# Kernel optimization log

Hardware: AMD Instinct MI355X
Metric: run time of the kernel (lower is better)

The kernel has to match this reference:

```python
import jax, jax.numpy as jnp
import numpy as np
from jax import lax

DT = 1.0 / 120.0
B, T = 4096, 128
TWO_PI = 2.0 * np.pi


def setup_inputs() -> dict:
    key = jax.random.key(0)
    k1, k2, k3, k4 = jax.random.split(key, 4)
    return {
        "params": jax.random.normal(k1, (4,), jnp.float32),
        "covariance_params": jax.random.normal(k2, (7,), jnp.float32),
        "init_states": jax.random.normal(k3, (B, 6), jnp.float32),
        "measurements": jax.random.normal(k4, (B, T, 3), jnp.float32),
    }


def _wrap(a):
    # wrap angle innovation to [-pi, pi]
    return a - TWO_PI * jnp.round(a / TWO_PI)


def _smooth_loss(params, covariance_params, init_state, z):
    # z: [T, 3] measurements of (x, y, theta)
    friction = (jnp.tanh(params[0]) + 1.0) * 0.01
    damping = (jnp.tanh(params[1]) + 1.0) * 0.01
    cp = jax.nn.sigmoid(covariance_params)
    R = jnp.diag(cp[:3])                                    # [3,3] meas noise
    Q = jnp.diag(cp[jnp.array([3, 3, 4, 4, 5, 6])])         # [6,6] proc noise
    I6 = jnp.eye(6, dtype=z.dtype)
    Hm = jnp.zeros((3, 6), z.dtype).at[0, 0].set(1.).at[1, 1].set(1.).at[2, 4].set(1.)
    P0 = 0.01 * I6

    def f_and_F(s):
        # free-sliding puck dynamics: [x, y, dx, dy, th, dth]
        x, y, dx, dy, th, dth = s
        ndx = dx - DT * (damping * dx + friction * jnp.tanh(100. * dx))
        ndy = dy - DT * (damping * dy + friction * jnp.tanh(100. * dy))
        ndth = dth * (1.0 - DT * damping)
        ns = jnp.stack([x + DT * dx, y + DT * dy, ndx, ndy, th + DT * dth, ndth])
        gx = 1.0 - DT * (damping + friction * 100. * (1. - jnp.tanh(100. * dx) ** 2))
        gy = 1.0 - DT * (damping + friction * 100. * (1. - jnp.tanh(100. * dy) ** 2))
        F = (I6.at[0, 2].set(DT).at[1, 3].set(DT).at[4, 5].set(DT)
               .at[2, 2].set(gx).at[3, 3].set(gy).at[5, 5].set(1.0 - DT * damping))
        return ns, F

    def ekf_step(carry, zt):
        s, P = carry
        sp, F = f_and_F(s)
        Pp = F @ P @ F.T + Q
        S = Hm @ Pp @ Hm.T + R
        innov = zt - Hm @ sp
        innov = innov.at[2].set(_wrap(innov[2]))
        K = jnp.linalg.solve(S, Hm @ Pp).T          # Pp H^T S^-1
        s_new = sp + K @ innov
        P_new = (I6 - K @ Hm) @ Pp
        return (s_new, P_new), (s_new, P_new, sp, Pp, F)

    _, (sf, Pf, sp, Pp, Fs) = lax.scan(ekf_step, (init_state, P0), z)

    # RTS backward pass
    def rts_step(carry, inp):
        s_next, P_next = carry
        s_f, P_f, sp_n, Pp_n, F_n = inp
        G = jnp.linalg.solve(Pp_n, F_n @ P_f).T     # P_f F^T Pp^{-1}
        s_s = s_f + G @ (s_next - sp_n)
        P_s = P_f + G @ (P_next - Pp_n) @ G.T
        return (s_s, P_s), (s_s, P_s)

    inp = (sf[:-1], Pf[:-1], sp[1:], Pp[1:], Fs[1:])
    _, (s_sm_head, P_sm_head) = lax.scan(rts_step, (sf[-1], Pf[-1]), inp, reverse=True)
    s_sm = jnp.concatenate([s_sm_head, sf[-1:]], 0)   # [T,6]
    P_sm = jnp.concatenate([P_sm_head, Pf[-1:]], 0)   # [T,6,6]

    # log-lik style loss vs measurements[2:] (as in compute_loss)
    zz, st, Pt = z[2:], s_sm[2:], P_sm[2:]
    Sv = jnp.einsum('ij,tjk,lk->til', Hm, Pt, Hm) + R  # [T-2,3,3] meas-space var
    innov_xy = zz[:, :2] - st[:, :2]
    a = zz[:, 2] - st[:, 4]
    a = jnp.where(a > 1.5 * np.pi, a - TWO_PI, a)
    a = jnp.where(a < -1.5 * np.pi, a + TWO_PI, a)
    innov = jnp.concatenate([innov_xy, a[:, None]], 1)
    sign, logdet = jnp.linalg.slogdet(Sv)
    return jnp.sum(sign * jnp.exp(logdet) + jnp.einsum('ti,tij,tj->t', innov, Sv, innov))


def reference(params, covariance_params, init_states, measurements):
    per_seg = jax.vmap(_smooth_loss, in_axes=(None, None, 0, 0))(
        params, covariance_params, init_states, measurements)
    return jnp.sum(per_seg)
```

## Files before the change

### kernel.cpp

```cpp
#include <hip/hip_runtime.h>
#include <cmath>


namespace {

constexpr int B = 4096;
constexpr int T = 128;
constexpr int SPB = 64;
constexpr int NBLK = B / SPB;
constexpr int NTH = 3 * SPB;
constexpr int NT = B * 3;
constexpr float DTc     = 1.0f / 120.0f;
constexpr float TWO_PIc = 6.28318530717958647692f;
constexpr float PI_1_5  = 4.71238898038468985769f;
constexpr float INV_2PI = 0.15915494309189533577f;

__device__ __forceinline__ float frcp(float x) { return __builtin_amdgcn_rcpf(x); }

__device__ __forceinline__ float fast_tanh(float x) {
  float e = __expf(2.0f * x);
  return 1.0f - 2.0f * frcp(e + 1.0f);
}
__device__ __forceinline__ float sigmoidf(float x) {
  return frcp(1.0f + __expf(-x));
}

__global__ __launch_bounds__(NTH, 1) void fused_kernel(
    const float* __restrict__ params, const float* __restrict__ covp,
    const float* __restrict__ init_states, const float* __restrict__ z,
    float4* __restrict__ hist4, float* __restrict__ hist1,
    float2* __restrict__ aq, float* __restrict__ out) {
  const int tid = threadIdx.x;
  const int f = tid >> 6;
  const int sb = tid & 63;
  const int blk = blockIdx.x;
  const int seq = blk * SPB + sb;
  const int gid = blk * NTH + tid;

  __shared__ float zl[384 * 65];
  __shared__ float red[3];

  {
    const float* __restrict__ zslab = z + (size_t)blk * SPB * (T * 3);
    const int q = (tid >= 96) ? 1 : 0;
    const int col = (tid - q * 96) * 4;
#pragma unroll 4
    for (int i = 0; i < 32; i++) {
      const int s2 = i * 2 + q;
      const float4 v4 = *(const float4*)(zslab + (size_t)i * 768 + tid * 4);
      zl[(col + 0) * 65 + s2] = v4.x;
      zl[(col + 1) * 65 + s2] = v4.y;
      zl[(col + 2) * 65 + s2] = v4.z;
      zl[(col + 3) * 65 + s2] = v4.w;
    }
  }
  __syncthreads();

  const float friction = (fast_tanh(params[0]) + 1.0f) * 0.01f;
  const float damping  = (fast_tanh(params[1]) + 1.0f) * 0.01f;
  float cp[7];
#pragma unroll
  for (int i = 0; i < 7; i++) cp[i] = sigmoidf(covp[i]);
  const float dcoef = 1.0f - DTc * damping;
  const bool isTH = (f == 2);
  const float q0 = isTH ? cp[5] : cp[3];
  const float q1 = isTH ? cp[6] : cp[4];
  const float r  = cp[f];

  const int pidx = (f == 0) ? 0 : (f == 1) ? 1 : 4;
  const int vidx = (f == 0) ? 2 : (f == 1) ? 3 : 5;
  float p = init_states[seq * 6 + pidx];
  float v = init_states[seq * 6 + vidx];
  float P00 = 0.01f, P01 = 0.0f, P11 = 0.01f;

#pragma unroll 8
  for (int t = 0; t < T; t++) {
    const float zc = zl[(t * 3 + f) * 65 + sb];

    float g, tv;
    if (!isTH) {
      const float th = fast_tanh(100.0f * v);
      tv = v - DTc * (damping * v + friction * th);
      g = 1.0f - DTc * (damping + 100.0f * friction * (1.0f - th * th));
    } else {
      tv = dcoef * v;
      g = dcoef;
    }
    const float tp = p + DTc * v;
    const float u = P01 + DTc * P11;
    const float Pp00 = P00 + DTc * P01 + DTc * u + q0;
    const float Pp01 = g * u;
    const float Pp11 = g * (g * P11) + q1;
    const float iS = frcp(Pp00 + r);
    const float K0 = Pp00 * iS;
    const float K1 = Pp01 * iS;
    float e = zc - tp;
    if (isTH) e = e - TWO_PIc * rintf(e * INV_2PI);
    p = tp + K0 * e;
    v = tv + K1 * e;
    const float om = 1.0f - K0;
    P00 = om * Pp00;
    P01 = om * Pp01;
    P11 = Pp11 - K1 * Pp01;

    hist4[(size_t)t * NT + gid] = make_float4(p, v, P00, P01);
    hist1[(size_t)t * NT + gid] = P11;
  }

  {
    const float zlv = zl[((T - 1) * 3 + f) * 65 + sb];
    float e = zlv - p;
    if (isTH) {
      if (e >  PI_1_5) e -= TWO_PIc;
      if (e < -PI_1_5) e += TWO_PIc;
    }
    const float a = P00 + r;
    aq[(size_t)(T - 1) * NT + gid] = make_float2(a, a * e * e);
  }

  float sp_ = p, sv_ = v, Ps00 = P00, Ps01 = P01, Ps11 = P11;

  float4 h4b[8];
  float h1b[8];
#pragma unroll
  for (int i = 0; i < 8; i++) {
    const int n2 = 126 - i;
    h4b[i] = hist4[(size_t)n2 * NT + gid];
    h1b[i] = hist1[(size_t)n2 * NT + gid];
  }

#pragma unroll 8
  for (int i = 0; i < 128; i++) {
    const int n = 126 - i;
    const int sl = i & 7;
    const float4 h4 = h4b[sl];
    const float h1 = h1b[sl];
    const int nz = (n < 2) ? 2 : n;
    const float zn_ = zl[(nz * 3 + f) * 65 + sb];
    const int nf = (n >= 10) ? (n - 8) : 2;
    h4b[sl] = hist4[(size_t)nf * NT + gid];
    h1b[sl] = hist1[(size_t)nf * NT + gid];

    const float fp = h4.x, fv = h4.y, f00 = h4.z, f01 = h4.w, f11 = h1;

    float g, tv;
    if (!isTH) {
      const float th = fast_tanh(100.0f * fv);
      tv = fv - DTc * (damping * fv + friction * th);
      g = 1.0f - DTc * (damping + 100.0f * friction * (1.0f - th * th));
    } else {
      tv = dcoef * fv;
      g = dcoef;
    }
    const float tp = fp + DTc * fv;
    const float u = f01 + DTc * f11;
    const float Pp00 = f00 + DTc * f01 + DTc * u + q0;
    const float Pp01 = g * u;
    const float Pp11 = g * (g * f11) + q1;

    const float idet = frcp(Pp00 * Pp11 - Pp01 * Pp01);
    const float W00 = f00, W01 = DTc * f00 + g * f01;
    const float W10 = f01, W11 = DTc * f01 + g * f11;
    const float G00 = (W00 * Pp11 - W01 * Pp01) * idet;
    const float G01 = (W01 * Pp00 - W00 * Pp01) * idet;
    const float G10 = (W10 * Pp11 - W11 * Pp01) * idet;
    const float G11 = (W11 * Pp00 - W10 * Pp01) * idet;

    const float ds0 = sp_ - tp, ds1 = sv_ - tv;
    const float np = fp + G00 * ds0 + G01 * ds1;
    const float nv = fv + G10 * ds0 + G11 * ds1;

    const float M00 = Ps00 - Pp00, M01 = Ps01 - Pp01, M11 = Ps11 - Pp11;
    const float GM00 = G00 * M00 + G01 * M01, GM01 = G00 * M01 + G01 * M11;
    const float GM10 = G10 * M00 + G11 * M01, GM11 = G10 * M01 + G11 * M11;
    Ps00 = f00 + GM00 * G00 + GM01 * G01;
    Ps01 = f01 + GM00 * G10 + GM01 * G11;
    Ps11 = f11 + GM10 * G10 + GM11 * G11;
    sp_ = np;
    sv_ = nv;

    if (n >= 2) {
      const float a = Ps00 + r;
      float e = zn_ - np;
      if (isTH) {
        if (e >  PI_1_5) e -= TWO_PIc;
        if (e < -PI_1_5) e += TWO_PIc;
      }
      aq[(size_t)n * NT + gid] = make_float2(a, a * e * e);
    }
  }

  __syncthreads();

  float part = 0.0f;
  const int base = blk * NTH;

  float2 b0[4], b1[4], b2[4];
#pragma unroll
  for (int k = 0; k < 4; k++) {
    const int pi = tid + k * NTH;
    const size_t o = (size_t)(2 + (pi >> 6)) * NT + base + (pi & 63);
    b0[k] = aq[o];
    b1[k] = aq[o + 64];
    b2[k] = aq[o + 128];
  }

#pragma unroll 4
  for (int k = 0; k < 44; k++) {
    const int sl = k & 3;
    const float2 x0 = b0[sl];
    const float2 x1 = b1[sl];
    const float2 x2 = b2[sl];
    const int kf = (k + 4 < 42) ? (k + 4) : 41;
    {
      const int pi = tid + kf * NTH;
      const size_t o = (size_t)(2 + (pi >> 6)) * NT + base + (pi & 63);
      b0[sl] = aq[o];
      b1[sl] = aq[o + 64];
      b2[sl] = aq[o + 128];
    }
    if (k < 42) part += x0.x * x1.x * x2.x + (x0.y + x1.y + x2.y);
  }

#pragma unroll
  for (int off = 32; off > 0; off >>= 1) part += __shfl_down(part, off);
  if ((tid & 63) == 0) red[tid >> 6] = part;
  __syncthreads();
  if (tid == 0) atomicAdd(out, red[0] + red[1] + red[2]);
}

}

extern "C" void kernel_launch(void* const* d_in, const int* in_sizes, int n_in,
                              void* d_out, int out_size, void* d_ws, size_t ws_size,
                              hipStream_t stream) {
  const float* params      = (const float*)d_in[0];
  const float* covp        = (const float*)d_in[1];
  const float* init_states = (const float*)d_in[2];
  const float* z           = (const float*)d_in[3];
  float* out = (float*)d_out;

  const size_t hist4B = (size_t)T * NT * sizeof(float4);
  const size_t hist1B = (size_t)T * NT * sizeof(float);
  const size_t aqB    = (size_t)T * NT * sizeof(float2);
  const size_t needBytes = hist4B + hist1B + aqB;

  hipMemsetAsync(d_out, 0, sizeof(float), stream);

  if (ws_size >= needBytes) {
    float4* hist4 = (float4*)d_ws;
    float*  hist1 = (float*)((char*)d_ws + hist4B);
    float2* aqp   = (float2*)((char*)d_ws + hist4B + hist1B);
    fused_kernel<<<NBLK, NTH, 0, stream>>>(params, covp, init_states, z,
                                           hist4, hist1, aqp, out);
  }
}
```

Before: 121.9 us.

## Split filter into one-wave blocks with LDS history and separate reduction kernel

Restructures the work so each 64-thread block handles one coordinate channel for 64 sequences, giving 192 blocks instead of 64. The float4 filter history now lives in shared memory rather than global workspace, and measurements are read straight from global memory instead of being transposed into LDS. The final loss reduction moves to a separate grid-stride kernel. The aim is better CU occupancy and less global history traffic, at the cost of an extra kernel launch, strided uncoalesced z reads, and 128 KB of LDS per block.

```diff
diff --git a/kernel.cpp b/kernel.cpp
--- a/kernel.cpp
+++ b/kernel.cpp
@@ -6,10 +6,12 @@
 
 constexpr int B = 4096;
 constexpr int T = 128;
-constexpr int SPB = 64;
-constexpr int NBLK = B / SPB;
-constexpr int NTH = 3 * SPB;
 constexpr int NT = B * 3;
+constexpr int CPB = 64;
+constexpr int NBLK = NT / CPB;
+constexpr int RBLK = 256;
+constexpr int RTH = 256;
+
 constexpr float DTc     = 1.0f / 120.0f;
 constexpr float TWO_PIc = 6.28318530717958647692f;
 constexpr float PI_1_5  = 4.71238898038468985769f;
@@ -25,36 +27,17 @@
   return frcp(1.0f + __expf(-x));
 }
 
-__global__ __launch_bounds__(NTH, 1) void fused_kernel(
+__global__ __launch_bounds__(CPB, 1) void filt_kernel(
     const float* __restrict__ params, const float* __restrict__ covp,
     const float* __restrict__ init_states, const float* __restrict__ z,
-    float4* __restrict__ hist4, float* __restrict__ hist1,
-    float2* __restrict__ aq, float* __restrict__ out) {
-  const int tid = threadIdx.x;
-  const int f = tid >> 6;
-  const int sb = tid & 63;
-  const int blk = blockIdx.x;
-  const int seq = blk * SPB + sb;
-  const int gid = blk * NTH + tid;
-
-  __shared__ float zl[384 * 65];
-  __shared__ float red[3];
-
-  {
-    const float* __restrict__ zslab = z + (size_t)blk * SPB * (T * 3);
-    const int q = (tid >= 96) ? 1 : 0;
-    const int col = (tid - q * 96) * 4;
-#pragma unroll 4
-    for (int i = 0; i < 32; i++) {
-      const int s2 = i * 2 + q;
-      const float4 v4 = *(const float4*)(zslab + (size_t)i * 768 + tid * 4);
-      zl[(col + 0) * 65 + s2] = v4.x;
-      zl[(col + 1) * 65 + s2] = v4.y;
-      zl[(col + 2) * 65 + s2] = v4.z;
-      zl[(col + 3) * 65 + s2] = v4.w;
-    }
-  }
-  __syncthreads();
+    float* __restrict__ hist1, float2* __restrict__ aq) {
+  const int lane = threadIdx.x;
+  const int blk  = blockIdx.x;
+  const int f    = blk >> 6;
+  const int seq  = ((blk & 63) << 6) + lane;
+  const int gid  = blk * CPB + lane;
+
+  __shared__ float4 h4s[T * CPB];
 
   const float friction = (fast_tanh(params[0]) + 1.0f) * 0.01f;
   const float damping  = (fast_tanh(params[1]) + 1.0f) * 0.01f;
@@ -73,9 +56,11 @@
   float v = init_states[seq * 6 + vidx];
   float P00 = 0.01f, P01 = 0.0f, P11 = 0.01f;
 
+  const float* __restrict__ zp = z + (size_t)seq * (T * 3) + f;
+
 #pragma unroll 8
   for (int t = 0; t < T; t++) {
-    const float zc = zl[(t * 3 + f) * 65 + sb];
+    const float zc = zp[t * 3];
 
     float g, tv;
     if (!isTH) {
@@ -103,45 +88,38 @@
     P01 = om * Pp01;
     P11 = Pp11 - K1 * Pp01;
 
-    hist4[(size_t)t * NT + gid] = make_float4(p, v, P00, P01);
+    h4s[t * CPB + lane] = make_float4(p, v, P00, P01);
     hist1[(size_t)t * NT + gid] = P11;
   }
 
   {
-    const float zlv = zl[((T - 1) * 3 + f) * 65 + sb];
-    float e = zlv - p;
+    float e = zp[(T - 1) * 3] - p;
     if (isTH) {
       if (e >  PI_1_5) e -= TWO_PIc;
       if (e < -PI_1_5) e += TWO_PIc;
     }
     const float a = P00 + r;
-    aq[(size_t)(T - 1) * NT + gid] = make_float2(a, a * e * e);
+    aq[((size_t)f * T + (T - 1)) * B + seq] = make_float2(a, a * e * e);
   }
 
   float sp_ = p, sv_ = v, Ps00 = P00, Ps01 = P01, Ps11 = P11;
 
-  float4 h4b[8];
   float h1b[8];
 #pragma unroll
-  for (int i = 0; i < 8; i++) {
-    const int n2 = 126 - i;
-    h4b[i] = hist4[(size_t)n2 * NT + gid];
-    h1b[i] = hist1[(size_t)n2 * NT + gid];
-  }
+  for (int i = 0; i < 8; i++) h1b[i] = hist1[(size_t)(126 - i) * NT + gid];
 
 #pragma unroll 8
   for (int i = 0; i < 128; i++) {
     const int n = 126 - i;
+    const int nc = (n < 2) ? 2 : n;
     const int sl = i & 7;
-    const float4 h4 = h4b[sl];
-    const float h1 = h1b[sl];
-    const int nz = (n < 2) ? 2 : n;
-    const float zn_ = zl[(nz * 3 + f) * 65 + sb];
+    const float4 h4 = h4s[nc * CPB + lane];
+    const float f11 = h1b[sl];
     const int nf = (n >= 10) ? (n - 8) : 2;
-    h4b[sl] = hist4[(size_t)nf * NT + gid];
     h1b[sl] = hist1[(size_t)nf * NT + gid];
-
-    const float fp = h4.x, fv = h4.y, f00 = h4.z, f01 = h4.w, f11 = h1;
+    const float zn_ = zp[nc * 3];
+
+    const float fp = h4.x, fv = h4.y, f00 = h4.z, f01 = h4.w;
 
     float g, tv;
     if (!isTH) {
@@ -186,47 +164,35 @@
         if (e >  PI_1_5) e -= TWO_PIc;
         if (e < -PI_1_5) e += TWO_PIc;
       }
-      aq[(size_t)n * NT + gid] = make_float2(a, a * e * e);
-    }
-  }
-
-  __syncthreads();
-
+      aq[((size_t)f * T + n) * B + seq] = make_float2(a, a * e * e);
+    }
+  }
+}
+
+__global__ __launch_bounds__(RTH) void reduce_kernel(
+    const float2* __restrict__ aq, float* __restrict__ out) {
+  const int tid = threadIdx.x;
+  constexpr int NTERM = 126 * B;
   float part = 0.0f;
-  const int base = blk * NTH;
-
-  float2 b0[4], b1[4], b2[4];
-#pragma unroll
-  for (int k = 0; k < 4; k++) {
-    const int pi = tid + k * NTH;
-    const size_t o = (size_t)(2 + (pi >> 6)) * NT + base + (pi & 63);
-    b0[k] = aq[o];
-    b1[k] = aq[o + 64];
-    b2[k] = aq[o + 128];
-  }
-
-#pragma unroll 4
-  for (int k = 0; k < 44; k++) {
-    const int sl = k & 3;
-    const float2 x0 = b0[sl];
-    const float2 x1 = b1[sl];
-    const float2 x2 = b2[sl];
-    const int kf = (k + 4 < 42) ? (k + 4) : 41;
-    {
-      const int pi = tid + kf * NTH;
-      const size_t o = (size_t)(2 + (pi >> 6)) * NT + base + (pi & 63);
-      b0[sl] = aq[o];
-      b1[sl] = aq[o + 64];
-      b2[sl] = aq[o + 128];
-    }
-    if (k < 42) part += x0.x * x1.x * x2.x + (x0.y + x1.y + x2.y);
-  }
-
+  for (int idx = blockIdx.x * RTH + tid; idx < NTERM; idx += RTH * RBLK) {
+    const int t = 2 + (idx >> 12);
+    const int s = idx & (B - 1);
+    const float2 a0 = aq[((size_t)0 * T + t) * B + s];
+    const float2 a1 = aq[((size_t)1 * T + t) * B + s];
+    const float2 a2 = aq[((size_t)2 * T + t) * B + s];
+    part += a0.x * a1.x * a2.x + (a0.y + a1.y + a2.y);
+  }
 #pragma unroll
   for (int off = 32; off > 0; off >>= 1) part += __shfl_down(part, off);
+  __shared__ float red[RTH / 64];
   if ((tid & 63) == 0) red[tid >> 6] = part;
   __syncthreads();
-  if (tid == 0) atomicAdd(out, red[0] + red[1] + red[2]);
+  if (tid == 0) {
+    float s = 0.0f;
+#pragma unroll
+    for (int w = 0; w < RTH / 64; w++) s += red[w];
+    atomicAdd(out, s);
+  }
 }
 
 }
@@ -240,18 +206,17 @@
   const float* z           = (const float*)d_in[3];
   float* out = (float*)d_out;
 
-  const size_t hist4B = (size_t)T * NT * sizeof(float4);
   const size_t hist1B = (size_t)T * NT * sizeof(float);
   const size_t aqB    = (size_t)T * NT * sizeof(float2);
-  const size_t needBytes = hist4B + hist1B + aqB;
+  const size_t needBytes = hist1B + aqB;
 
   hipMemsetAsync(d_out, 0, sizeof(float), stream);
 
   if (ws_size >= needBytes) {
-    float4* hist4 = (float4*)d_ws;
-    float*  hist1 = (float*)((char*)d_ws + hist4B);
-    float2* aqp   = (float2*)((char*)d_ws + hist4B + hist1B);
-    fused_kernel<<<NBLK, NTH, 0, stream>>>(params, covp, init_states, z,
-                                           hist4, hist1, aqp, out);
-  }
-}
+    float*  hist1 = (float*)d_ws;
+    float2* aqp   = (float2*)((char*)d_ws + hist1B);
+    filt_kernel<<<NBLK, CPB, 0, stream>>>(params, covp, init_states, z,
+                                          hist1, aqp);
+    reduce_kernel<<<RBLK, RTH, 0, stream>>>(aqp, out);
+  }
+}
```

Result: slower. 134.5 us (+10.3%).
